# Optimization experiments

Hardware: AMD Instinct MI355X
Metric: run time of the kernel (lower is better)

The kernel has to match this reference:

```python
import jax, jax.numpy as jnp
import numpy as np

N_GENES = 15135
N_CMT = 1000
HID = 64


def _gcn_norm(edge_index, n):
    # add self-loops, compute symmetric normalization deg^-1/2 * deg^-1/2
    loop = jnp.arange(n, dtype=edge_index.dtype)
    src = jnp.concatenate([edge_index[0], loop])
    dst = jnp.concatenate([edge_index[1], loop])
    deg = jax.ops.segment_sum(jnp.ones_like(src, dtype=jnp.float32), dst, num_segments=n)
    dinv = jnp.where(deg > 0, 1.0 / jnp.sqrt(deg), 0.0)
    return src, dst, dinv[src] * dinv[dst]


def _gcn_conv(x, W, b, src, dst, norm, n):
    h = x @ W                                  # [bs, N, H]
    m = h[:, src, :] * norm[None, :, None]     # gather messages [bs, E, H]
    out = jnp.zeros_like(h).at[:, dst, :].add(m)
    return out + b


def setup_inputs():
    key = jax.random.key(0)
    ks = jax.random.split(key, 16)
    bs, nf, hfc, ncls, E, P = 8, 64, 128, 2, 242160, 120000
    s = 0.05
    return {
        "x": jax.random.normal(ks[0], (bs, N_GENES, nf), jnp.float32),
        "batch": jnp.zeros((bs,), jnp.int32),
        "edge_index": jax.random.randint(ks[1], (2, E), 0, N_GENES),
        "path_row": jax.random.randint(ks[2], (P,), 0, N_GENES),
        "path_col": jax.random.randint(ks[3], (P,), 0, N_CMT),
        "W1": jax.random.normal(ks[4], (nf, HID), jnp.float32) * s,
        "b1": jnp.zeros((HID,), jnp.float32),
        "W2": jax.random.normal(ks[5], (HID, HID), jnp.float32) * s,
        "b2": jnp.zeros((HID,), jnp.float32),
        "W3": jax.random.normal(ks[6], (HID, HID), jnp.float32) * s,
        "b3": jnp.zeros((HID,), jnp.float32),
        "fcW": jax.random.normal(ks[7], (3 * HID, 1), jnp.float32) * s,
        "fcb": jnp.zeros((1,), jnp.float32),
        "l1W": jax.random.normal(ks[8], (N_CMT, hfc), jnp.float32) * s,
        "l1b": jnp.zeros((hfc,), jnp.float32),
        "l2W": jax.random.normal(ks[9], (hfc, ncls), jnp.float32) * s,
        "l2b": jnp.zeros((ncls,), jnp.float32),
    }


def reference(x, batch, edge_index, path_row, path_col,
              W1, b1, W2, b2, W3, b3, fcW, fcb, l1W, l1b, l2W, l2b):
    bs, n = x.shape[0], x.shape[1]
    src, dst, norm = _gcn_norm(edge_index, n)

    x1 = jax.nn.relu(_gcn_conv(x, W1, b1, src, dst, norm, n))
    x2 = jax.nn.relu(_gcn_conv(x1, W2, b2, src, dst, norm, n))
    x3 = jax.nn.relu(_gcn_conv(x2, W3, b3, src, dst, norm, n))
    # mode='cat': torch.stack(xs, -1).view(bs, N, -1) -> layout [..., h*L + l]
    xc = jnp.stack([x1, x2, x3], axis=-1).reshape(bs, n, HID * 3)

    # pathway pooling: scatter_mean(x[row], col) over node axis
    xt = jnp.transpose(xc, (1, 0, 2))            # [N, bs, F]
    g = xt[path_row]                             # [P, bs, F]
    sums = jax.ops.segment_sum(g, path_col, num_segments=N_CMT)
    cnt = jax.ops.segment_sum(jnp.ones_like(path_col, dtype=xc.dtype), path_col, num_segments=N_CMT)
    pooled = sums / jnp.maximum(cnt, 1.0)[:, None, None]   # [n_cmt, bs, F]
    pooled = jnp.transpose(pooled, (1, 0, 2)).reshape(-1, HID * 3)  # [bs*n_cmt, F]

    h = (pooled @ fcW + fcb).reshape(bs, N_CMT)   # fc -> view(-1, n_cmt)
    h = jax.nn.relu(h @ l1W + l1b)                # (dropout is identity in eval)
    h = h @ l2W + l2b
    return jax.nn.log_softmax(h, axis=-1)
```

## Files before the change

kernel.cpp:

```cpp
#include <hip/hip_runtime.h>
#include <hip/hip_bf16.h>
#include <hip/hip_fp16.h>
#include <math.h>

#define HID 64

#if defined(__has_builtin)
#if __has_builtin(__builtin_amdgcn_cvt_pk_f32_fp8) && __has_builtin(__builtin_amdgcn_cvt_pk_fp8_f32)
#define HWFP8 1
#endif
#endif

typedef float vfloat2 __attribute__((ext_vector_type(2)));
typedef __attribute__((ext_vector_type(8))) short short8_t;
typedef __attribute__((ext_vector_type(4))) float f32x4;

union ABFrag { short8_t s; unsigned short u[8]; };


__device__ __forceinline__ unsigned short f2bf(float x) {
    unsigned int u = __float_as_uint(x);
    unsigned int r = u + 0x7fffu + ((u >> 16) & 1u);
    return (unsigned short)(r >> 16);
}

#ifndef HWFP8
__device__ __forceinline__ unsigned int enc8_sw(float a) {
    unsigned short hb = __half_as_ushort(__float2half(a));
    unsigned int r = (unsigned int)hb + 0x7fu + ((hb >> 8) & 1u);
    return (r >> 8) & 0xffu;
}
__device__ __forceinline__ float dec8_sw(unsigned int b) {
    return __half2float(__ushort_as_half((unsigned short)(b << 8)));
}
#endif

__device__ __forceinline__ unsigned int enc4(float a, float b, float c, float d) {
#ifdef HWFP8
    int r = __builtin_amdgcn_cvt_pk_fp8_f32(a, b, 0, false);
    r = __builtin_amdgcn_cvt_pk_fp8_f32(c, d, r, true);
    return (unsigned int)r;
#else
    return enc8_sw(a) | (enc8_sw(b) << 8) | (enc8_sw(c) << 16) | (enc8_sw(d) << 24);
#endif
}

__device__ __forceinline__ void dec4(unsigned int w, float* f) {
#ifdef HWFP8
    vfloat2 a = __builtin_amdgcn_cvt_pk_f32_fp8((int)w, false);
    vfloat2 b = __builtin_amdgcn_cvt_pk_f32_fp8((int)w, true);
    f[0] = a.x; f[1] = a.y; f[2] = b.x; f[3] = b.y;
#else
    f[0] = dec8_sw(w & 0xffu); f[1] = dec8_sw((w >> 8) & 0xffu);
    f[2] = dec8_sw((w >> 16) & 0xffu); f[3] = dec8_sw(w >> 24);
#endif
}

__device__ __forceinline__ void dec8(uint2 g, float* f) {
    dec4(g.x, f);
    dec4(g.y, f + 4);
}


__global__ __launch_bounds__(256) void k_pre_count(const int* __restrict__ edst, int* __restrict__ deg, int E,
                                                   const int* __restrict__ pcol, int* __restrict__ ccnt, int P,
                                                   const float* __restrict__ W1, const float* __restrict__ W2,
                                                   const float* __restrict__ W3, unsigned short* __restrict__ Wt) {
    int gth = blockIdx.x * blockDim.x + threadIdx.x;
    int GT = gridDim.x * blockDim.x;
    for (int e = gth; e < E; e += GT) atomicAdd(&deg[edst[e]], 1);
    for (int p = gth; p < P; p += GT) atomicAdd(&ccnt[pcol[p]], 1);
    for (int i = gth; i < 3 * 4096; i += GT) {
        int l = i >> 12, r = i & 4095;
        int k = r >> 6, c = r & 63;
        const float* W = (l == 0) ? W1 : (l == 1) ? W2 : W3;
        Wt[(l << 12) + c * 64 + k] = f2bf(W[r]);
    }
}

__global__ __launch_bounds__(256) void k_pre_scan(const int* __restrict__ deg, int* __restrict__ rowoff, int N,
                                                  const int* __restrict__ ccnt, int* __restrict__ coff, int NC,
                                                  float* __restrict__ dinv) {
    __shared__ int part[256];
    int t = threadIdx.x;
    int gth = blockIdx.x * blockDim.x + t;
    int GT = gridDim.x * blockDim.x;
    for (int i = gth; i < N; i += GT) dinv[i] = rsqrtf((float)(deg[i] + 1));

    const int* cnt = nullptr; int* off = nullptr; int n = 0;
    if (blockIdx.x == 0)      { cnt = deg;  off = rowoff; n = N; }
    else if (blockIdx.x == 1) { cnt = ccnt; off = coff;   n = NC; }
    else return;

    int CH = (n + 255) >> 8;
    int lo = min(t * CH, n), hi = min(lo + CH, n);
    int sum = 0;
    for (int i = lo; i < hi; ++i) sum += cnt[i];
    part[t] = sum;
    __syncthreads();
    for (int o = 1; o < 256; o <<= 1) {
        int v = (t >= o) ? part[t - o] : 0;
        __syncthreads();
        part[t] += v;
        __syncthreads();
    }
    int run = (t == 0) ? 0 : part[t - 1];
    for (int i = lo; i < hi; ++i) { off[i] = run; run += cnt[i]; }
    if (t == 255) off[n] = run;
}

__global__ __launch_bounds__(256) void k_pre_scatter(const int* __restrict__ esrc, const int* __restrict__ edst,
                                                     const float* __restrict__ dinv, const int* __restrict__ rowoff,
                                                     int* __restrict__ fill, int* __restrict__ ssrc,
                                                     float* __restrict__ snorm, int E,
                                                     const int* __restrict__ prow, const int* __restrict__ pcol,
                                                     const int* __restrict__ coff, int* __restrict__ cfill,
                                                     int* __restrict__ crow, int P) {
    int gth = blockIdx.x * blockDim.x + threadIdx.x;
    int GT = gridDim.x * blockDim.x;
    for (int e = gth; e < E; e += GT) {
        int s = esrc[e], d = edst[e];
        int pos = rowoff[d] + atomicAdd(&fill[d], 1);
        ssrc[pos]  = s;
        snorm[pos] = dinv[s] * dinv[d];
    }
    for (int p = gth; p < P; p += GT) {
        int c = pcol[p];
        int pos = coff[c] + atomicAdd(&cfill[c], 1);
        crow[pos] = prow[p];
    }
}


template<int MODE>
__global__ __launch_bounds__(256) void k_gemm_mfma(const void* __restrict__ Xv,
                                                   const unsigned short* __restrict__ Wt,
                                                   unsigned int* __restrict__ Yq,
                                                   float S, int N, int rowsTot) {
    __shared__ float sOut[4][16 * 68];
    int t = threadIdx.x;
    int w = t >> 6, lane = t & 63;
    int r0w = blockIdx.x * 64 + w * 16;
    int rA = r0w + (lane & 15);
    int kg = (lane >> 4) * 8;
    int cc = lane & 15;

    const float* Xf = (const float*)Xv;
    const unsigned short* Xh = (const unsigned short*)Xv;

    f32x4 acc[4] = {f32x4{}, f32x4{}, f32x4{}, f32x4{}};

#pragma unroll
    for (int k0 = 0; k0 < 64; k0 += 32) {
        ABFrag a;
        if (rA < rowsTot) {
            if (MODE == 0) {
                int n = rA >> 3, b = rA & 7;
                const float* p = &Xf[((size_t)b * N + n) * 64 + k0 + kg];
                float4 v0 = *(const float4*)p;
                float4 v1 = *(const float4*)(p + 4);
                a.u[0] = f2bf(v0.x); a.u[1] = f2bf(v0.y);
                a.u[2] = f2bf(v0.z); a.u[3] = f2bf(v0.w);
                a.u[4] = f2bf(v1.x); a.u[5] = f2bf(v1.y);
                a.u[6] = f2bf(v1.z); a.u[7] = f2bf(v1.w);
            } else {
                a.s = *(const short8_t*)&Xh[(size_t)rA * 64 + k0 + kg];
            }
        } else {
#pragma unroll
            for (int j = 0; j < 8; ++j) a.u[j] = 0;
        }
#pragma unroll
        for (int c = 0; c < 4; ++c) {
            ABFrag b;
            b.s = *(const short8_t*)&Wt[(size_t)(c * 16 + cc) * 64 + k0 + kg];
            acc[c] = __builtin_amdgcn_mfma_f32_16x16x32_bf16(a.s, b.s, acc[c], 0, 0, 0);
        }
    }

    float* so = &sOut[w][0];
    int cr = (lane >> 4) * 4;
#pragma unroll
    for (int c = 0; c < 4; ++c) {
        so[(cr + 0) * 68 + c * 16 + cc] = acc[c][0];
        so[(cr + 1) * 68 + c * 16 + cc] = acc[c][1];
        so[(cr + 2) * 68 + c * 16 + cc] = acc[c][2];
        so[(cr + 3) * 68 + c * 16 + cc] = acc[c][3];
    }
    __syncthreads();
#pragma unroll
    for (int i = 0; i < 4; ++i) {
        int idx = lane + i * 64;
        int row = idx >> 4, ci = idx & 15;
        int grow = r0w + row;
        if (grow < rowsTot) {
            float4 v = *(const float4*)&so[row * 68 + ci * 4];
            Yq[(size_t)grow * 16 + ci] =
                enc4(v.x * S, v.y * S, v.z * S, v.w * S);
        }
    }
}

template<int LAYER, bool STORE>
__global__ __launch_bounds__(256) void k_agg(const uint2* __restrict__ Y,
                                             const int* __restrict__ rowoff,
                                             const int* __restrict__ ssrc,
                                             const float* __restrict__ snorm,
                                             const float* __restrict__ dinv,
                                             const float* __restrict__ bias,
                                             const float* __restrict__ fcW,
                                             uint4* __restrict__ O,
                                             float* __restrict__ sArr,
                                             float invS, int N) {
    int n = blockIdx.x * 4 + (threadIdx.x >> 6);
    if (n >= N) return;
    int lane = threadIdx.x & 63;
    int hb = (lane & 7) * 8;
    float bv[8], wv[8];
#pragma unroll
    for (int k = 0; k < 8; ++k) { bv[k] = bias[hb + k]; wv[k] = fcW[3 * (hb + k) + LAYER]; }

    float dn = dinv[n];
    float w0 = dn * dn;
    float acc[8], f[8];
    dec8(Y[(size_t)n * 64 + lane], f);
#pragma unroll
    for (int k = 0; k < 8; ++k) acc[k] = w0 * f[k];

    int beg = rowoff[n], end = rowoff[n + 1];
    int i = beg;
    for (; i + 7 < end; i += 8) {
        int   sI[8];
        float wI[8];
        uint2 g[8];
#pragma unroll
        for (int u = 0; u < 8; ++u) { sI[u] = ssrc[i + u]; wI[u] = snorm[i + u]; }
#pragma unroll
        for (int u = 0; u < 8; ++u) g[u] = Y[(size_t)sI[u] * 64 + lane];
#pragma unroll
        for (int u = 0; u < 8; ++u) {
            dec8(g[u], f);
#pragma unroll
            for (int k = 0; k < 8; ++k) acc[k] = fmaf(wI[u], f[k], acc[k]);
        }
    }
    for (; i < end; ++i) {
        int s = ssrc[i];
        float w = snorm[i];
        dec8(Y[(size_t)s * 64 + lane], f);
#pragma unroll
        for (int k = 0; k < 8; ++k) acc[k] = fmaf(w, f[k], acc[k]);
    }

    float sv = 0.f;
#pragma unroll
    for (int k = 0; k < 8; ++k) {
        float o = fmaxf(fmaf(acc[k], invS, bv[k]), 0.f);
        acc[k] = o;
        sv = fmaf(o, wv[k], sv);
    }
    if (STORE) {
        uint4 o;
        o.x = (unsigned int)f2bf(acc[0]) | ((unsigned int)f2bf(acc[1]) << 16);
        o.y = (unsigned int)f2bf(acc[2]) | ((unsigned int)f2bf(acc[3]) << 16);
        o.z = (unsigned int)f2bf(acc[4]) | ((unsigned int)f2bf(acc[5]) << 16);
        o.w = (unsigned int)f2bf(acc[6]) | ((unsigned int)f2bf(acc[7]) << 16);
        O[(size_t)n * 64 + lane] = o;
    }
    sv += __shfl_down(sv, 4, 64);
    sv += __shfl_down(sv, 2, 64);
    sv += __shfl_down(sv, 1, 64);
    if ((lane & 7) == 0) {
        int b = lane >> 3;
        float* sp = sArr + (size_t)n * 8 + b;
        if (LAYER == 0) *sp = sv;
        else            *sp += sv;
    }
}


__global__ __launch_bounds__(64) void k_poolg(const float* __restrict__ sArr,
                                              const int* __restrict__ coff,
                                              const int* __restrict__ crow,
                                              float* __restrict__ hpoolT) {
    int c = blockIdx.x;
    int lane = threadIdx.x;
    int beg = coff[c], end = coff[c + 1];
    int b = lane & 7;
    float acc = 0.f;
    int i = beg + (lane >> 3);
    for (; i + 24 < end; i += 32) {
        int r0 = crow[i], r1 = crow[i + 8], r2 = crow[i + 16], r3 = crow[i + 24];
        float a0 = sArr[(size_t)r0 * 8 + b];
        float a1 = sArr[(size_t)r1 * 8 + b];
        float a2 = sArr[(size_t)r2 * 8 + b];
        float a3 = sArr[(size_t)r3 * 8 + b];
        acc += (a0 + a1) + (a2 + a3);
    }
    for (; i < end; i += 8) acc += sArr[(size_t)crow[i] * 8 + b];
    acc += __shfl_down(acc, 32, 64);
    acc += __shfl_down(acc, 16, 64);
    acc += __shfl_down(acc, 8, 64);
    if (lane < 8) {
        float inv = 1.f / fmaxf((float)(end - beg), 1.f);
        hpoolT[(size_t)c * 8 + b] = acc * inv;
    }
}

__global__ __launch_bounds__(128) void k_l1f(const float* __restrict__ hpoolT,
                                             const float* __restrict__ fcb,
                                             const float* __restrict__ l1W,
                                             float* __restrict__ hpre,
                                             int* __restrict__ done,
                                             const float* __restrict__ l1b,
                                             const float* __restrict__ l2W,
                                             const float* __restrict__ l2b,
                                             float* __restrict__ out,
                                             int NC, int HFC, int bs, int NCLS,
                                             int CHUNK, int nBlocks) {
    __shared__ float hl[64];
    int b = blockIdx.y;
    int c0 = blockIdx.x * CHUNK;
    int j = threadIdx.x;
    int cend = min(c0 + CHUNK, NC);
    for (int c = c0 + j; c < cend; c += blockDim.x)
        hl[c - c0] = hpoolT[(size_t)c * 8 + b] + fcb[0];
    __syncthreads();
    float acc = 0.f;
    for (int c = c0; c < cend; ++c) acc = fmaf(hl[c - c0], l1W[(size_t)c * HFC + j], acc);
    atomicAdd(&hpre[(size_t)b * HFC + j], acc);

    __threadfence();
    __syncthreads();
    __shared__ int amLast;
    if (j == 0) amLast = (atomicAdd(done, 1) == nBlocks - 1);
    __syncthreads();
    if (!amLast) return;
    __threadfence();

    __shared__ float sZ[64];
    int g = j >> 3, l8 = j & 7;
    int nout = bs * NCLS;
    float v = 0.f;
    int b2 = g / NCLS, k2 = g - b2 * NCLS;
    if (g < nout) {
        for (int jj = l8; jj < HFC; jj += 8) {
            float h = fmaxf(hpre[(size_t)b2 * HFC + jj] + l1b[jj], 0.f);
            v = fmaf(h, l2W[(size_t)jj * NCLS + k2], v);
        }
    }
    v += __shfl_down(v, 4, 8);
    v += __shfl_down(v, 2, 8);
    v += __shfl_down(v, 1, 8);
    if (l8 == 0 && g < nout) sZ[g] = v + l2b[k2];
    __syncthreads();
    if (j < bs) {
        float m = -1e30f;
        for (int c = 0; c < NCLS; ++c) m = fmaxf(m, sZ[j * NCLS + c]);
        float s = 0.f;
        for (int c = 0; c < NCLS; ++c) s += expf(sZ[j * NCLS + c] - m);
        float lse = m + logf(s);
        for (int c = 0; c < NCLS; ++c) out[j * NCLS + c] = sZ[j * NCLS + c] - lse;
    }
}


extern "C" void kernel_launch(void* const* d_in, const int* in_sizes, int n_in,
                              void* d_out, int out_size, void* d_ws, size_t ws_size,
                              hipStream_t stream) {
    const float* x   = (const float*)d_in[0];
    const int* eidx  = (const int*)d_in[2];
    const int* prow  = (const int*)d_in[3];
    const int* pcol  = (const int*)d_in[4];
    const float* W1  = (const float*)d_in[5];
    const float* b1  = (const float*)d_in[6];
    const float* W2  = (const float*)d_in[7];
    const float* b2  = (const float*)d_in[8];
    const float* W3  = (const float*)d_in[9];
    const float* b3  = (const float*)d_in[10];
    const float* fcW = (const float*)d_in[11];
    const float* fcb = (const float*)d_in[12];
    const float* l1W = (const float*)d_in[13];
    const float* l1b = (const float*)d_in[14];
    const float* l2W = (const float*)d_in[15];
    const float* l2b = (const float*)d_in[16];
    float* out = (float*)d_out;

    const int bs   = in_sizes[1];
    const int E    = in_sizes[2] / 2;
    const int P    = in_sizes[3];
    const int N    = in_sizes[0] / (bs * HID);
    const int HFC  = in_sizes[14];
    const int NC   = in_sizes[13] / HFC;
    const int NCLS = in_sizes[15] / HFC;
    const int rows = N * bs;

    const int* esrc = eidx;
    const int* edst = eidx + E;

    size_t off = 0;
    auto alloc = [&](size_t bytes) -> void* {
        void* r = (char*)d_ws + off;
        off += (bytes + 255) & ~(size_t)255;
        return r;
    };
    char* zbase   = (char*)d_ws;
    int*   deg    = (int*)  alloc((size_t)N * 4);
    int*   fill   = (int*)  alloc((size_t)N * 4);
    int*   ccnt   = (int*)  alloc((size_t)NC * 4);
    int*   cfill  = (int*)  alloc((size_t)NC * 4);
    float* hpre   = (float*)alloc((size_t)bs * HFC * 4);
    int*   done   = (int*)  alloc(4);
    size_t zspan  = off;
    float* dinv   = (float*)alloc((size_t)N * 4);
    int*   rowoff = (int*)  alloc(((size_t)N + 1) * 4);
    int*   coff   = (int*)  alloc(((size_t)NC + 1) * 4);
    int*   crow   = (int*)  alloc((size_t)P * 4);
    float* hpoolT = (float*)alloc((size_t)NC * bs * 4);
    int*   ssrc   = (int*)  alloc((size_t)E * 4);
    float* snorm  = (float*)alloc((size_t)E * 4);
    unsigned int* Yq   = (unsigned int*)alloc((size_t)rows * HID);
    unsigned short* X1 = (unsigned short*)alloc((size_t)rows * HID * 2);
    unsigned short* X2 = (unsigned short*)alloc((size_t)rows * HID * 2);
    float* sArr   = (float*)alloc((size_t)rows * 4);
    unsigned short* Wt = (unsigned short*)alloc((size_t)3 * 64 * 64 * 2);

    hipMemsetAsync(zbase, 0, zspan, stream);

    int gPre = 512;
    k_pre_count<<<gPre, 256, 0, stream>>>(edst, deg, E, pcol, ccnt, P, W1, W2, W3, Wt);
    k_pre_scan<<<64, 256, 0, stream>>>(deg, rowoff, N, ccnt, coff, NC, dinv);
    k_pre_scatter<<<gPre, 256, 0, stream>>>(esrc, edst, dinv, rowoff, fill, ssrc, snorm, E,
                                            prow, pcol, coff, cfill, crow, P);

    const float S1 = 1.f,  iS1 = 1.f;
    const float S2 = 16.f, iS2 = 1.f / 16.f;
    const float S3 = 128.f, iS3 = 1.f / 128.f;

    int gG = (rows + 63) / 64;
    int gA = (N + 3) / 4;
    k_gemm_mfma<0><<<gG, 256, 0, stream>>>(x, Wt, Yq, S1, N, rows);
    k_agg<0, true><<<gA, 256, 0, stream>>>((const uint2*)Yq, rowoff, ssrc, snorm, dinv, b1, fcW, (uint4*)X1, sArr, iS1, N);
    k_gemm_mfma<1><<<gG, 256, 0, stream>>>(X1, Wt + 4096, Yq, S2, N, rows);
    k_agg<1, true><<<gA, 256, 0, stream>>>((const uint2*)Yq, rowoff, ssrc, snorm, dinv, b2, fcW, (uint4*)X2, sArr, iS2, N);
    k_gemm_mfma<1><<<gG, 256, 0, stream>>>(X2, Wt + 8192, Yq, S3, N, rows);
    k_agg<2, false><<<gA, 256, 0, stream>>>((const uint2*)Yq, rowoff, ssrc, snorm, dinv, b3, fcW, nullptr, sArr, iS3, N);

    k_poolg<<<NC, 64, 0, stream>>>(sArr, coff, crow, hpoolT);

    const int CHUNK = 40;
    dim3 gL1((NC + CHUNK - 1) / CHUNK, bs);
    int nBlocks = gL1.x * gL1.y;
    k_l1f<<<gL1, 128, 0, stream>>>(hpoolT, fcb, l1W, hpre, done, l1b, l2W, l2b, out,
                                   NC, HFC, bs, NCLS, CHUNK, nBlocks);
}
```

Before: 361.1 us.

## Fuse whole pipeline into one cooperative persistent kernel with grid syncs

Replaces the chain of separate launches (preprocessing count/scan/scatter, three GEMM and aggregation layers, pooling, MLP head) with one cooperative kernel that uses grid.sync between phases and grid-stride loops over tiles. The goal is to remove per-launch overhead and the idle gaps between many small kernels. The trade-offs are that each grid barrier has its own cost, the scan phases now run on only two blocks, and the persistent grid of at most 1024 blocks may give less parallelism or occupancy than the original launches. If the cooperative launch fails, the code falls back to the old multi-kernel path.

```diff
diff --git a/kernel.cpp b/kernel.cpp
--- a/kernel.cpp
+++ b/kernel.cpp
@@ -1,7 +1,10 @@
 #include <hip/hip_runtime.h>
+#include <hip/hip_cooperative_groups.h>
 #include <hip/hip_bf16.h>
 #include <hip/hip_fp16.h>
 #include <math.h>
+
+namespace cg = cooperative_groups;
 
 #define HID 64
 
@@ -59,6 +62,332 @@
 __device__ __forceinline__ void dec8(uint2 g, float* f) {
     dec4(g.x, f);
     dec4(g.y, f + 4);
+}
+
+
+struct MegaArgs {
+    const float* x;
+    const int* esrc; const int* edst;
+    const int* prow; const int* pcol;
+    const float* W1; const float* W2; const float* W3;
+    const float* b1; const float* b2; const float* b3;
+    const float* fcW; const float* fcb;
+    const float* l1W; const float* l1b;
+    const float* l2W; const float* l2b;
+    float* out;
+    int* deg; int* fill; int* ccnt; int* cfill;
+    float* hpre; float* dinv;
+    int* rowoff; int* coff; int* crow;
+    float* hpoolT; int* ssrc; float* snorm;
+    unsigned int* Yq; unsigned short* X1; unsigned short* X2;
+    float* sArr; unsigned short* Wt;
+    int N, E, P, NC, HFC, bs, NCLS, rows;
+};
+
+template<int MODE>
+__device__ __forceinline__ void gemm_phase(float* sOutAll, const void* Xv,
+                                           const unsigned short* Wt,
+                                           unsigned int* Yq, float S,
+                                           int N, int rowsTot,
+                                           int bid, int nB, int tid) {
+    int w = tid >> 6, lane = tid & 63;
+    int nT = (rowsTot + 63) >> 6;
+    const float* Xf = (const float*)Xv;
+    const unsigned short* Xh = (const unsigned short*)Xv;
+    float* so = sOutAll + w * (16 * 68);
+    int cc = lane & 15;
+    int kg = (lane >> 4) * 8;
+    int cr = (lane >> 4) * 4;
+
+    for (int tile = bid; tile < nT; tile += nB) {
+        int r0w = tile * 64 + w * 16;
+        int rA = r0w + (lane & 15);
+        f32x4 acc[4] = {f32x4{}, f32x4{}, f32x4{}, f32x4{}};
+#pragma unroll
+        for (int k0 = 0; k0 < 64; k0 += 32) {
+            ABFrag a;
+            if (rA < rowsTot) {
+                if (MODE == 0) {
+                    int n = rA >> 3, b = rA & 7;
+                    const float* p = &Xf[((size_t)b * N + n) * 64 + k0 + kg];
+                    float4 v0 = *(const float4*)p;
+                    float4 v1 = *(const float4*)(p + 4);
+                    a.u[0] = f2bf(v0.x); a.u[1] = f2bf(v0.y);
+                    a.u[2] = f2bf(v0.z); a.u[3] = f2bf(v0.w);
+                    a.u[4] = f2bf(v1.x); a.u[5] = f2bf(v1.y);
+                    a.u[6] = f2bf(v1.z); a.u[7] = f2bf(v1.w);
+                } else {
+                    a.s = *(const short8_t*)&Xh[(size_t)rA * 64 + k0 + kg];
+                }
+            } else {
+#pragma unroll
+                for (int j = 0; j < 8; ++j) a.u[j] = 0;
+            }
+#pragma unroll
+            for (int c = 0; c < 4; ++c) {
+                ABFrag b;
+                b.s = *(const short8_t*)&Wt[(size_t)(c * 16 + cc) * 64 + k0 + kg];
+                acc[c] = __builtin_amdgcn_mfma_f32_16x16x32_bf16(a.s, b.s, acc[c], 0, 0, 0);
+            }
+        }
+#pragma unroll
+        for (int c = 0; c < 4; ++c) {
+            so[(cr + 0) * 68 + c * 16 + cc] = acc[c][0];
+            so[(cr + 1) * 68 + c * 16 + cc] = acc[c][1];
+            so[(cr + 2) * 68 + c * 16 + cc] = acc[c][2];
+            so[(cr + 3) * 68 + c * 16 + cc] = acc[c][3];
+        }
+        __syncthreads();
+#pragma unroll
+        for (int i = 0; i < 4; ++i) {
+            int idx = lane + i * 64;
+            int row = idx >> 4, ci = idx & 15;
+            int grow = r0w + row;
+            if (grow < rowsTot) {
+                float4 v = *(const float4*)&so[row * 68 + ci * 4];
+                Yq[(size_t)grow * 16 + ci] =
+                    enc4(v.x * S, v.y * S, v.z * S, v.w * S);
+            }
+        }
+        __syncthreads();
+    }
+}
+
+template<int LAYER, bool STORE>
+__device__ __forceinline__ void agg_phase(const uint2* Y, const int* rowoff,
+                                          const int* ssrc, const float* snorm,
+                                          const float* dinv, const float* bias,
+                                          const float* fcW, uint4* O, float* sArr,
+                                          float invS, int N,
+                                          int bid, int nB, int tid) {
+    int w = tid >> 6, lane = tid & 63;
+    int nG = (N + 3) >> 2;
+    int hb = (lane & 7) * 8;
+    float bv[8], wv[8];
+#pragma unroll
+    for (int k = 0; k < 8; ++k) { bv[k] = bias[hb + k]; wv[k] = fcW[3 * (hb + k) + LAYER]; }
+
+    for (int g = bid; g < nG; g += nB) {
+        int n = g * 4 + w;
+        if (n < N) {
+            float dn = dinv[n];
+            float w0 = dn * dn;
+            float acc[8], f[8];
+            dec8(Y[(size_t)n * 64 + lane], f);
+#pragma unroll
+            for (int k = 0; k < 8; ++k) acc[k] = w0 * f[k];
+
+            int beg = rowoff[n], end = rowoff[n + 1];
+            int i = beg;
+            for (; i + 7 < end; i += 8) {
+                int   sI[8];
+                float wI[8];
+                uint2 gg[8];
+#pragma unroll
+                for (int u = 0; u < 8; ++u) { sI[u] = ssrc[i + u]; wI[u] = snorm[i + u]; }
+#pragma unroll
+                for (int u = 0; u < 8; ++u) gg[u] = Y[(size_t)sI[u] * 64 + lane];
+#pragma unroll
+                for (int u = 0; u < 8; ++u) {
+                    dec8(gg[u], f);
+#pragma unroll
+                    for (int k = 0; k < 8; ++k) acc[k] = fmaf(wI[u], f[k], acc[k]);
+                }
+            }
+            for (; i < end; ++i) {
+                int s = ssrc[i];
+                float ww = snorm[i];
+                dec8(Y[(size_t)s * 64 + lane], f);
+#pragma unroll
+                for (int k = 0; k < 8; ++k) acc[k] = fmaf(ww, f[k], acc[k]);
+            }
+
+            float sv = 0.f;
+#pragma unroll
+            for (int k = 0; k < 8; ++k) {
+                float o = fmaxf(fmaf(acc[k], invS, bv[k]), 0.f);
+                acc[k] = o;
+                sv = fmaf(o, wv[k], sv);
+            }
+            if (STORE) {
+                uint4 o;
+                o.x = (unsigned int)f2bf(acc[0]) | ((unsigned int)f2bf(acc[1]) << 16);
+                o.y = (unsigned int)f2bf(acc[2]) | ((unsigned int)f2bf(acc[3]) << 16);
+                o.z = (unsigned int)f2bf(acc[4]) | ((unsigned int)f2bf(acc[5]) << 16);
+                o.w = (unsigned int)f2bf(acc[6]) | ((unsigned int)f2bf(acc[7]) << 16);
+                O[(size_t)n * 64 + lane] = o;
+            }
+            sv += __shfl_down(sv, 4, 64);
+            sv += __shfl_down(sv, 2, 64);
+            sv += __shfl_down(sv, 1, 64);
+            if ((lane & 7) == 0) {
+                int b = lane >> 3;
+                float* sp = sArr + (size_t)n * 8 + b;
+                if (LAYER == 0) *sp = sv;
+                else            *sp += sv;
+            }
+        }
+    }
+}
+
+union SmemU {
+    float sOut[4 * 16 * 68];
+    int   part[256];
+    float hl2[2][64];
+    float sZ[64];
+};
+
+__global__ __launch_bounds__(256, 4) void k_mega(MegaArgs A) {
+    cg::grid_group grid = cg::this_grid();
+    __shared__ SmemU sm;
+    int tid = threadIdx.x;
+    int bid = blockIdx.x;
+    int nB  = gridDim.x;
+    int GT  = nB * 256;
+    int gth = bid * 256 + tid;
+    int w = tid >> 6, lane = tid & 63;
+
+    for (int e = gth; e < A.E; e += GT) atomicAdd(&A.deg[A.edst[e]], 1);
+    for (int p = gth; p < A.P; p += GT) atomicAdd(&A.ccnt[A.pcol[p]], 1);
+    for (int i = gth; i < 3 * 4096; i += GT) {
+        int l = i >> 12, r = i & 4095;
+        int k = r >> 6, c = r & 63;
+        const float* W = (l == 0) ? A.W1 : (l == 1) ? A.W2 : A.W3;
+        A.Wt[(l << 12) + c * 64 + k] = f2bf(W[r]);
+    }
+    grid.sync();
+
+    for (int i = gth; i < A.N; i += GT) A.dinv[i] = rsqrtf((float)(A.deg[i] + 1));
+    if (bid < 2) {
+        const int* cnt; int* off; int n;
+        if (bid == 0) { cnt = A.deg;  off = A.rowoff; n = A.N; }
+        else          { cnt = A.ccnt; off = A.coff;   n = A.NC; }
+        int t = tid;
+        int CH = (n + 255) >> 8;
+        int lo = min(t * CH, n), hi = min(lo + CH, n);
+        int sum = 0;
+        for (int i = lo; i < hi; ++i) sum += cnt[i];
+        sm.part[t] = sum;
+        __syncthreads();
+        for (int o = 1; o < 256; o <<= 1) {
+            int v = (t >= o) ? sm.part[t - o] : 0;
+            __syncthreads();
+            sm.part[t] += v;
+            __syncthreads();
+        }
+        int run = (t == 0) ? 0 : sm.part[t - 1];
+        for (int i = lo; i < hi; ++i) { off[i] = run; run += cnt[i]; }
+        if (t == 255) off[n] = run;
+    }
+    grid.sync();
+
+    for (int e = gth; e < A.E; e += GT) {
+        int s = A.esrc[e], d = A.edst[e];
+        int pos = A.rowoff[d] + atomicAdd(&A.fill[d], 1);
+        A.ssrc[pos]  = s;
+        A.snorm[pos] = A.dinv[s] * A.dinv[d];
+    }
+    for (int p = gth; p < A.P; p += GT) {
+        int c = A.pcol[p];
+        int pos = A.coff[c] + atomicAdd(&A.cfill[c], 1);
+        A.crow[pos] = A.prow[p];
+    }
+    grid.sync();
+
+    const float S1 = 1.f,   iS1 = 1.f;
+    const float S2 = 16.f,  iS2 = 1.f / 16.f;
+    const float S3 = 128.f, iS3 = 1.f / 128.f;
+
+    gemm_phase<0>(sm.sOut, A.x, A.Wt, A.Yq, S1, A.N, A.rows, bid, nB, tid);
+    grid.sync();
+    agg_phase<0, true>((const uint2*)A.Yq, A.rowoff, A.ssrc, A.snorm, A.dinv, A.b1, A.fcW,
+                       (uint4*)A.X1, A.sArr, iS1, A.N, bid, nB, tid);
+    grid.sync();
+    gemm_phase<1>(sm.sOut, A.X1, A.Wt + 4096, A.Yq, S2, A.N, A.rows, bid, nB, tid);
+    grid.sync();
+    agg_phase<1, true>((const uint2*)A.Yq, A.rowoff, A.ssrc, A.snorm, A.dinv, A.b2, A.fcW,
+                       (uint4*)A.X2, A.sArr, iS2, A.N, bid, nB, tid);
+    grid.sync();
+    gemm_phase<1>(sm.sOut, A.X2, A.Wt + 8192, A.Yq, S3, A.N, A.rows, bid, nB, tid);
+    grid.sync();
+    agg_phase<2, false>((const uint2*)A.Yq, A.rowoff, A.ssrc, A.snorm, A.dinv, A.b3, A.fcW,
+                        nullptr, A.sArr, iS3, A.N, bid, nB, tid);
+    grid.sync();
+
+    for (int c = bid * 4 + w; c < A.NC; c += nB * 4) {
+        int beg = A.coff[c], end = A.coff[c + 1];
+        int b = lane & 7;
+        float acc = 0.f;
+        int i = beg + (lane >> 3);
+        for (; i + 24 < end; i += 32) {
+            int r0 = A.crow[i], r1 = A.crow[i + 8], r2 = A.crow[i + 16], r3 = A.crow[i + 24];
+            float a0 = A.sArr[(size_t)r0 * 8 + b];
+            float a1 = A.sArr[(size_t)r1 * 8 + b];
+            float a2 = A.sArr[(size_t)r2 * 8 + b];
+            float a3 = A.sArr[(size_t)r3 * 8 + b];
+            acc += (a0 + a1) + (a2 + a3);
+        }
+        for (; i < end; i += 8) acc += A.sArr[(size_t)A.crow[i] * 8 + b];
+        acc += __shfl_down(acc, 32, 64);
+        acc += __shfl_down(acc, 16, 64);
+        acc += __shfl_down(acc, 8, 64);
+        if (lane < 8) {
+            float inv = 1.f / fmaxf((float)(end - beg), 1.f);
+            A.hpoolT[(size_t)c * 8 + b] = acc * inv;
+        }
+    }
+    grid.sync();
+
+    {
+        const int CHUNK = 40;
+        int gx25 = (A.NC + CHUNK - 1) / CHUNK;
+        int nJobs = gx25 * A.bs;
+        int h = tid >> 7, j = tid & 127;
+        float fcb0 = A.fcb[0];
+        for (int jj = bid * 2; jj < nJobs; jj += nB * 2) {
+            int J = jj + h;
+            int gx = J % gx25, b = J / gx25;
+            int c0 = gx * CHUNK;
+            int cend = min(c0 + CHUNK, A.NC);
+            float* hl = sm.hl2[h];
+            for (int c = c0 + j; c < cend; c += 128)
+                hl[c - c0] = A.hpoolT[(size_t)c * 8 + b] + fcb0;
+            __syncthreads();
+            float acc = 0.f;
+            for (int c = c0; c < cend; ++c)
+                acc = fmaf(hl[c - c0], A.l1W[(size_t)c * A.HFC + j], acc);
+            atomicAdd(&A.hpre[(size_t)b * A.HFC + j], acc);
+            __syncthreads();
+        }
+    }
+    grid.sync();
+
+    if (bid == 0) {
+        int j = tid;
+        int g = j >> 3, l8 = j & 7;
+        int nout = A.bs * A.NCLS;
+        float v = 0.f;
+        int b2 = g / A.NCLS, k2 = g - b2 * A.NCLS;
+        if (g < nout) {
+            for (int jj2 = l8; jj2 < A.HFC; jj2 += 8) {
+                float hh = fmaxf(A.hpre[(size_t)b2 * A.HFC + jj2] + A.l1b[jj2], 0.f);
+                v = fmaf(hh, A.l2W[(size_t)jj2 * A.NCLS + k2], v);
+            }
+        }
+        v += __shfl_down(v, 4, 8);
+        v += __shfl_down(v, 2, 8);
+        v += __shfl_down(v, 1, 8);
+        if (l8 == 0 && g < nout) sm.sZ[g] = v + A.l2b[k2];
+        __syncthreads();
+        if (j < A.bs) {
+            float m = -1e30f;
+            for (int c = 0; c < A.NCLS; ++c) m = fmaxf(m, sm.sZ[j * A.NCLS + c]);
+            float s = 0.f;
+            for (int c = 0; c < A.NCLS; ++c) s += expf(sm.sZ[j * A.NCLS + c] - m);
+            float lse = m + logf(s);
+            for (int c = 0; c < A.NCLS; ++c) A.out[j * A.NCLS + c] = sm.sZ[j * A.NCLS + c] - lse;
+        }
+    }
 }
 
 
@@ -131,74 +460,13 @@
     }
 }
 
-
 template<int MODE>
 __global__ __launch_bounds__(256) void k_gemm_mfma(const void* __restrict__ Xv,
                                                    const unsigned short* __restrict__ Wt,
                                                    unsigned int* __restrict__ Yq,
                                                    float S, int N, int rowsTot) {
     __shared__ float sOut[4][16 * 68];
-    int t = threadIdx.x;
-    int w = t >> 6, lane = t & 63;
-    int r0w = blockIdx.x * 64 + w * 16;
-    int rA = r0w + (lane & 15);
-    int kg = (lane >> 4) * 8;
-    int cc = lane & 15;
-
-    const float* Xf = (const float*)Xv;
-    const unsigned short* Xh = (const unsigned short*)Xv;
-
-    f32x4 acc[4] = {f32x4{}, f32x4{}, f32x4{}, f32x4{}};
-
-#pragma unroll
-    for (int k0 = 0; k0 < 64; k0 += 32) {
-        ABFrag a;
-        if (rA < rowsTot) {
-            if (MODE == 0) {
-                int n = rA >> 3, b = rA & 7;
-                const float* p = &Xf[((size_t)b * N + n) * 64 + k0 + kg];
-                float4 v0 = *(const float4*)p;
-                float4 v1 = *(const float4*)(p + 4);
-                a.u[0] = f2bf(v0.x); a.u[1] = f2bf(v0.y);
-                a.u[2] = f2bf(v0.z); a.u[3] = f2bf(v0.w);
-                a.u[4] = f2bf(v1.x); a.u[5] = f2bf(v1.y);
-                a.u[6] = f2bf(v1.z); a.u[7] = f2bf(v1.w);
-            } else {
-                a.s = *(const short8_t*)&Xh[(size_t)rA * 64 + k0 + kg];
-            }
-        } else {
-#pragma unroll
-            for (int j = 0; j < 8; ++j) a.u[j] = 0;
-        }
-#pragma unroll
-        for (int c = 0; c < 4; ++c) {
-            ABFrag b;
-            b.s = *(const short8_t*)&Wt[(size_t)(c * 16 + cc) * 64 + k0 + kg];
-            acc[c] = __builtin_amdgcn_mfma_f32_16x16x32_bf16(a.s, b.s, acc[c], 0, 0, 0);
-        }
-    }
-
-    float* so = &sOut[w][0];
-    int cr = (lane >> 4) * 4;
-#pragma unroll
-    for (int c = 0; c < 4; ++c) {
-        so[(cr + 0) * 68 + c * 16 + cc] = acc[c][0];
-        so[(cr + 1) * 68 + c * 16 + cc] = acc[c][1];
-        so[(cr + 2) * 68 + c * 16 + cc] = acc[c][2];
-        so[(cr + 3) * 68 + c * 16 + cc] = acc[c][3];
-    }
-    __syncthreads();
-#pragma unroll
-    for (int i = 0; i < 4; ++i) {
-        int idx = lane + i * 64;
-        int row = idx >> 4, ci = idx & 15;
-        int grow = r0w + row;
-        if (grow < rowsTot) {
-            float4 v = *(const float4*)&so[row * 68 + ci * 4];
-            Yq[(size_t)grow * 16 + ci] =
-                enc4(v.x * S, v.y * S, v.z * S, v.w * S);
-        }
-    }
+    gemm_phase<MODE>(&sOut[0][0], Xv, Wt, Yq, S, N, rowsTot, blockIdx.x, gridDim.x, threadIdx.x);
 }
 
 template<int LAYER, bool STORE>
@@ -212,72 +480,9 @@
                                              uint4* __restrict__ O,
                                              float* __restrict__ sArr,
                                              float invS, int N) {
-    int n = blockIdx.x * 4 + (threadIdx.x >> 6);
-    if (n >= N) return;
-    int lane = threadIdx.x & 63;
-    int hb = (lane & 7) * 8;
-    float bv[8], wv[8];
-#pragma unroll
-    for (int k = 0; k < 8; ++k) { bv[k] = bias[hb + k]; wv[k] = fcW[3 * (hb + k) + LAYER]; }
-
-    float dn = dinv[n];
-    float w0 = dn * dn;
-    float acc[8], f[8];
-    dec8(Y[(size_t)n * 64 + lane], f);
-#pragma unroll
-    for (int k = 0; k < 8; ++k) acc[k] = w0 * f[k];
-
-    int beg = rowoff[n], end = rowoff[n + 1];
-    int i = beg;
-    for (; i + 7 < end; i += 8) {
-        int   sI[8];
-        float wI[8];
-        uint2 g[8];
-#pragma unroll
-        for (int u = 0; u < 8; ++u) { sI[u] = ssrc[i + u]; wI[u] = snorm[i + u]; }
-#pragma unroll
-        for (int u = 0; u < 8; ++u) g[u] = Y[(size_t)sI[u] * 64 + lane];
-#pragma unroll
-        for (int u = 0; u < 8; ++u) {
-            dec8(g[u], f);
-#pragma unroll
-            for (int k = 0; k < 8; ++k) acc[k] = fmaf(wI[u], f[k], acc[k]);
-        }
-    }
-    for (; i < end; ++i) {
-        int s = ssrc[i];
-        float w = snorm[i];
-        dec8(Y[(size_t)s * 64 + lane], f);
-#pragma unroll
-        for (int k = 0; k < 8; ++k) acc[k] = fmaf(w, f[k], acc[k]);
-    }
-
-    float sv = 0.f;
-#pragma unroll
-    for (int k = 0; k < 8; ++k) {
-        float o = fmaxf(fmaf(acc[k], invS, bv[k]), 0.f);
-        acc[k] = o;
-        sv = fmaf(o, wv[k], sv);
-    }
-    if (STORE) {
-        uint4 o;
-        o.x = (unsigned int)f2bf(acc[0]) | ((unsigned int)f2bf(acc[1]) << 16);
-        o.y = (unsigned int)f2bf(acc[2]) | ((unsigned int)f2bf(acc[3]) << 16);
-        o.z = (unsigned int)f2bf(acc[4]) | ((unsigned int)f2bf(acc[5]) << 16);
-        o.w = (unsigned int)f2bf(acc[6]) | ((unsigned int)f2bf(acc[7]) << 16);
-        O[(size_t)n * 64 + lane] = o;
-    }
-    sv += __shfl_down(sv, 4, 64);
-    sv += __shfl_down(sv, 2, 64);
-    sv += __shfl_down(sv, 1, 64);
-    if ((lane & 7) == 0) {
-        int b = lane >> 3;
-        float* sp = sArr + (size_t)n * 8 + b;
-        if (LAYER == 0) *sp = sv;
-        else            *sp += sv;
-    }
-}
-
+    agg_phase<LAYER, STORE>(Y, rowoff, ssrc, snorm, dinv, bias, fcW, O, sArr, invS, N,
+                            blockIdx.x, gridDim.x, threadIdx.x);
+}
 
 __global__ __launch_bounds__(64) void k_poolg(const float* __restrict__ sArr,
                                               const int* __restrict__ coff,
@@ -427,6 +632,29 @@
 
     hipMemsetAsync(zbase, 0, zspan, stream);
 
+    MegaArgs A;
+    A.x = x; A.esrc = esrc; A.edst = edst; A.prow = prow; A.pcol = pcol;
+    A.W1 = W1; A.W2 = W2; A.W3 = W3; A.b1 = b1; A.b2 = b2; A.b3 = b3;
+    A.fcW = fcW; A.fcb = fcb; A.l1W = l1W; A.l1b = l1b; A.l2W = l2W; A.l2b = l2b;
+    A.out = out;
+    A.deg = deg; A.fill = fill; A.ccnt = ccnt; A.cfill = cfill;
+    A.hpre = hpre; A.dinv = dinv; A.rowoff = rowoff; A.coff = coff; A.crow = crow;
+    A.hpoolT = hpoolT; A.ssrc = ssrc; A.snorm = snorm;
+    A.Yq = Yq; A.X1 = X1; A.X2 = X2; A.sArr = sArr; A.Wt = Wt;
+    A.N = N; A.E = E; A.P = P; A.NC = NC; A.HFC = HFC; A.bs = bs; A.NCLS = NCLS; A.rows = rows;
+
+    int maxB = 0;
+    hipError_t occErr = hipOccupancyMaxActiveBlocksPerMultiprocessor(&maxB, k_mega, 256, 0);
+    if (occErr != hipSuccess || maxB < 1) maxB = 1;
+    int nB = maxB * 256;
+    if (nB > 1024) nB = 1024;
+    if (nB < 2) nB = 2;
+
+    void* kargs[] = { (void*)&A };
+    hipError_t err = hipLaunchCooperativeKernel((const void*)k_mega, dim3(nB), dim3(256),
+                                                kargs, 0, stream);
+    if (err == hipSuccess) return;
+
     int gPre = 512;
     k_pre_count<<<gPre, 256, 0, stream>>>(edst, deg, E, pcol, ccnt, P, W1, W2, W3, Wt);
     k_pre_scan<<<64, 256, 0, stream>>>(deg, rowoff, N, ccnt, coff, NC, dinv);
```

New measurement: 984.8 us. 173% more time.

## Fuse layer-1 GEMM with preprocessing and fold pooling into L1 kernel

Applied to the files above, without the earlier changes.

The layer-1 GEMM, which depends only on x and W1, now runs in the same launch as the degree and count atomics and the W2/W3 transpose. It uses extra blocks and reads W1 directly with on-the-fly bf16 conversion. The pathway mean-pooling kernel is removed and its work moves into the first FC kernel, where each 16-lane group pools one pathway into shared memory. This cuts two kernel launches and the hpoolT round trip, but pooling is now repeated per batch-column block, and W1 is loaded strided and uncached-transposed per block.

```diff
diff --git a/kernel.cpp b/kernel.cpp
--- a/kernel.cpp
+++ b/kernel.cpp
@@ -61,22 +61,146 @@
     dec4(g.y, f + 4);
 }
 
-
-__global__ __launch_bounds__(256) void k_pre_count(const int* __restrict__ edst, int* __restrict__ deg, int E,
-                                                   const int* __restrict__ pcol, int* __restrict__ ccnt, int P,
-                                                   const float* __restrict__ W1, const float* __restrict__ W2,
-                                                   const float* __restrict__ W3, unsigned short* __restrict__ Wt) {
-    int gth = blockIdx.x * blockDim.x + threadIdx.x;
-    int GT = gridDim.x * blockDim.x;
-    for (int e = gth; e < E; e += GT) atomicAdd(&deg[edst[e]], 1);
-    for (int p = gth; p < P; p += GT) atomicAdd(&ccnt[pcol[p]], 1);
-    for (int i = gth; i < 3 * 4096; i += GT) {
-        int l = i >> 12, r = i & 4095;
-        int k = r >> 6, c = r & 63;
-        const float* W = (l == 0) ? W1 : (l == 1) ? W2 : W3;
-        Wt[(l << 12) + c * 64 + k] = f2bf(W[r]);
-    }
-}
+__device__ __forceinline__ void gemm_bf16_phase(float* so4, const unsigned short* Xh,
+                                                const unsigned short* Wt,
+                                                unsigned int* Yq, float S,
+                                                int rowsTot, int tile, int tid) {
+    int w = tid >> 6, lane = tid & 63;
+    float* so = so4 + w * (16 * 68);
+    int cc = lane & 15;
+    int kg = (lane >> 4) * 8;
+    int cr = (lane >> 4) * 4;
+    int r0w = tile * 64 + w * 16;
+    int rA = r0w + (lane & 15);
+    f32x4 acc[4] = {f32x4{}, f32x4{}, f32x4{}, f32x4{}};
+#pragma unroll
+    for (int k0 = 0; k0 < 64; k0 += 32) {
+        ABFrag a;
+        if (rA < rowsTot) {
+            a.s = *(const short8_t*)&Xh[(size_t)rA * 64 + k0 + kg];
+        } else {
+#pragma unroll
+            for (int j = 0; j < 8; ++j) a.u[j] = 0;
+        }
+#pragma unroll
+        for (int c = 0; c < 4; ++c) {
+            ABFrag b;
+            b.s = *(const short8_t*)&Wt[(size_t)(c * 16 + cc) * 64 + k0 + kg];
+            acc[c] = __builtin_amdgcn_mfma_f32_16x16x32_bf16(a.s, b.s, acc[c], 0, 0, 0);
+        }
+    }
+#pragma unroll
+    for (int c = 0; c < 4; ++c) {
+        so[(cr + 0) * 68 + c * 16 + cc] = acc[c][0];
+        so[(cr + 1) * 68 + c * 16 + cc] = acc[c][1];
+        so[(cr + 2) * 68 + c * 16 + cc] = acc[c][2];
+        so[(cr + 3) * 68 + c * 16 + cc] = acc[c][3];
+    }
+    __syncthreads();
+#pragma unroll
+    for (int i = 0; i < 4; ++i) {
+        int idx = lane + i * 64;
+        int row = idx >> 4, ci = idx & 15;
+        int grow = r0w + row;
+        if (grow < rowsTot) {
+            float4 v = *(const float4*)&so[row * 68 + ci * 4];
+            Yq[(size_t)grow * 16 + ci] =
+                enc4(v.x * S, v.y * S, v.z * S, v.w * S);
+        }
+    }
+}
+
+template<int DUMMY>
+__global__ __launch_bounds__(256) void k_gemm_mfma(const unsigned short* __restrict__ Xh,
+                                                   const unsigned short* __restrict__ Wt,
+                                                   unsigned int* __restrict__ Yq,
+                                                   float S, int rowsTot) {
+    __shared__ float sOut[4][16 * 68];
+    gemm_bf16_phase(&sOut[0][0], Xh, Wt, Yq, S, rowsTot, blockIdx.x, threadIdx.x);
+}
+
+__global__ __launch_bounds__(256) void k_fused1(const float* __restrict__ x,
+                                                const float* __restrict__ W1,
+                                                unsigned int* __restrict__ Yq,
+                                                float S, int N, int rowsTot, int gG,
+                                                const int* __restrict__ edst, int* __restrict__ deg, int E,
+                                                const int* __restrict__ pcol, int* __restrict__ ccnt, int P,
+                                                const float* __restrict__ W2, const float* __restrict__ W3,
+                                                unsigned short* __restrict__ Wt) {
+    __shared__ float sOut[4][16 * 68];
+    int tid = threadIdx.x;
+    if ((int)blockIdx.x < gG) {
+        int w = tid >> 6, lane = tid & 63;
+        float* so = &sOut[w][0];
+        int cc = lane & 15;
+        int kg = (lane >> 4) * 8;
+        int cr = (lane >> 4) * 4;
+        int r0w = blockIdx.x * 64 + w * 16;
+        int rA = r0w + (lane & 15);
+        ABFrag a[2];
+#pragma unroll
+        for (int h = 0; h < 2; ++h) {
+            if (rA < rowsTot) {
+                int n = rA >> 3, b = rA & 7;
+                const float* p = &x[((size_t)b * N + n) * 64 + h * 32 + kg];
+                float4 v0 = *(const float4*)p;
+                float4 v1 = *(const float4*)(p + 4);
+                a[h].u[0] = f2bf(v0.x); a[h].u[1] = f2bf(v0.y);
+                a[h].u[2] = f2bf(v0.z); a[h].u[3] = f2bf(v0.w);
+                a[h].u[4] = f2bf(v1.x); a[h].u[5] = f2bf(v1.y);
+                a[h].u[6] = f2bf(v1.z); a[h].u[7] = f2bf(v1.w);
+            } else {
+#pragma unroll
+                for (int j = 0; j < 8; ++j) a[h].u[j] = 0;
+            }
+        }
+        f32x4 acc[4] = {f32x4{}, f32x4{}, f32x4{}, f32x4{}};
+#pragma unroll
+        for (int h = 0; h < 2; ++h) {
+#pragma unroll
+            for (int c = 0; c < 4; ++c) {
+                ABFrag b;
+#pragma unroll
+                for (int j = 0; j < 8; ++j)
+                    b.u[j] = f2bf(W1[(size_t)(h * 32 + kg + j) * 64 + c * 16 + cc]);
+                acc[c] = __builtin_amdgcn_mfma_f32_16x16x32_bf16(a[h].s, b.s, acc[c], 0, 0, 0);
+            }
+        }
+#pragma unroll
+        for (int c = 0; c < 4; ++c) {
+            so[(cr + 0) * 68 + c * 16 + cc] = acc[c][0];
+            so[(cr + 1) * 68 + c * 16 + cc] = acc[c][1];
+            so[(cr + 2) * 68 + c * 16 + cc] = acc[c][2];
+            so[(cr + 3) * 68 + c * 16 + cc] = acc[c][3];
+        }
+        __syncthreads();
+#pragma unroll
+        for (int i = 0; i < 4; ++i) {
+            int idx = lane + i * 64;
+            int row = idx >> 4, ci = idx & 15;
+            int grow = r0w + row;
+            if (grow < rowsTot) {
+                float4 v = *(const float4*)&so[row * 68 + ci * 4];
+                Yq[(size_t)grow * 16 + ci] =
+                    enc4(v.x * S, v.y * S, v.z * S, v.w * S);
+            }
+        }
+    } else {
+        int cb = blockIdx.x - gG;
+        int nCB = gridDim.x - gG;
+        int gth = cb * 256 + tid;
+        int GT = nCB * 256;
+        for (int e = gth; e < E; e += GT) atomicAdd(&deg[edst[e]], 1);
+        for (int p = gth; p < P; p += GT) atomicAdd(&ccnt[pcol[p]], 1);
+        for (int i = gth; i < 2 * 4096; i += GT) {
+            int l = i >> 12, r = i & 4095;
+            int k = r >> 6, c = r & 63;
+            const float* W = (l == 0) ? W2 : W3;
+            Wt[(l << 12) + c * 64 + k] = f2bf(W[r]);
+        }
+    }
+}
+
 
 __global__ __launch_bounds__(256) void k_pre_scan(const int* __restrict__ deg, int* __restrict__ rowoff, int N,
                                                   const int* __restrict__ ccnt, int* __restrict__ coff, int NC,
@@ -131,75 +255,6 @@
     }
 }
 
-
-template<int MODE>
-__global__ __launch_bounds__(256) void k_gemm_mfma(const void* __restrict__ Xv,
-                                                   const unsigned short* __restrict__ Wt,
-                                                   unsigned int* __restrict__ Yq,
-                                                   float S, int N, int rowsTot) {
-    __shared__ float sOut[4][16 * 68];
-    int t = threadIdx.x;
-    int w = t >> 6, lane = t & 63;
-    int r0w = blockIdx.x * 64 + w * 16;
-    int rA = r0w + (lane & 15);
-    int kg = (lane >> 4) * 8;
-    int cc = lane & 15;
-
-    const float* Xf = (const float*)Xv;
-    const unsigned short* Xh = (const unsigned short*)Xv;
-
-    f32x4 acc[4] = {f32x4{}, f32x4{}, f32x4{}, f32x4{}};
-
-#pragma unroll
-    for (int k0 = 0; k0 < 64; k0 += 32) {
-        ABFrag a;
-        if (rA < rowsTot) {
-            if (MODE == 0) {
-                int n = rA >> 3, b = rA & 7;
-                const float* p = &Xf[((size_t)b * N + n) * 64 + k0 + kg];
-                float4 v0 = *(const float4*)p;
-                float4 v1 = *(const float4*)(p + 4);
-                a.u[0] = f2bf(v0.x); a.u[1] = f2bf(v0.y);
-                a.u[2] = f2bf(v0.z); a.u[3] = f2bf(v0.w);
-                a.u[4] = f2bf(v1.x); a.u[5] = f2bf(v1.y);
-                a.u[6] = f2bf(v1.z); a.u[7] = f2bf(v1.w);
-            } else {
-                a.s = *(const short8_t*)&Xh[(size_t)rA * 64 + k0 + kg];
-            }
-        } else {
-#pragma unroll
-            for (int j = 0; j < 8; ++j) a.u[j] = 0;
-        }
-#pragma unroll
-        for (int c = 0; c < 4; ++c) {
-            ABFrag b;
-            b.s = *(const short8_t*)&Wt[(size_t)(c * 16 + cc) * 64 + k0 + kg];
-            acc[c] = __builtin_amdgcn_mfma_f32_16x16x32_bf16(a.s, b.s, acc[c], 0, 0, 0);
-        }
-    }
-
-    float* so = &sOut[w][0];
-    int cr = (lane >> 4) * 4;
-#pragma unroll
-    for (int c = 0; c < 4; ++c) {
-        so[(cr + 0) * 68 + c * 16 + cc] = acc[c][0];
-        so[(cr + 1) * 68 + c * 16 + cc] = acc[c][1];
-        so[(cr + 2) * 68 + c * 16 + cc] = acc[c][2];
-        so[(cr + 3) * 68 + c * 16 + cc] = acc[c][3];
-    }
-    __syncthreads();
-#pragma unroll
-    for (int i = 0; i < 4; ++i) {
-        int idx = lane + i * 64;
-        int row = idx >> 4, ci = idx & 15;
-        int grow = r0w + row;
-        if (grow < rowsTot) {
-            float4 v = *(const float4*)&so[row * 68 + ci * 4];
-            Yq[(size_t)grow * 16 + ci] =
-                enc4(v.x * S, v.y * S, v.z * S, v.w * S);
-        }
-    }
-}
 
 template<int LAYER, bool STORE>
 __global__ __launch_bounds__(256) void k_agg(const uint2* __restrict__ Y,
@@ -278,53 +333,40 @@
     }
 }
 
-
-__global__ __launch_bounds__(64) void k_poolg(const float* __restrict__ sArr,
-                                              const int* __restrict__ coff,
-                                              const int* __restrict__ crow,
-                                              float* __restrict__ hpoolT) {
-    int c = blockIdx.x;
-    int lane = threadIdx.x;
-    int beg = coff[c], end = coff[c + 1];
-    int b = lane & 7;
-    float acc = 0.f;
-    int i = beg + (lane >> 3);
-    for (; i + 24 < end; i += 32) {
-        int r0 = crow[i], r1 = crow[i + 8], r2 = crow[i + 16], r3 = crow[i + 24];
-        float a0 = sArr[(size_t)r0 * 8 + b];
-        float a1 = sArr[(size_t)r1 * 8 + b];
-        float a2 = sArr[(size_t)r2 * 8 + b];
-        float a3 = sArr[(size_t)r3 * 8 + b];
-        acc += (a0 + a1) + (a2 + a3);
-    }
-    for (; i < end; i += 8) acc += sArr[(size_t)crow[i] * 8 + b];
-    acc += __shfl_down(acc, 32, 64);
-    acc += __shfl_down(acc, 16, 64);
-    acc += __shfl_down(acc, 8, 64);
-    if (lane < 8) {
-        float inv = 1.f / fmaxf((float)(end - beg), 1.f);
-        hpoolT[(size_t)c * 8 + b] = acc * inv;
-    }
-}
-
-__global__ __launch_bounds__(128) void k_l1f(const float* __restrict__ hpoolT,
-                                             const float* __restrict__ fcb,
-                                             const float* __restrict__ l1W,
-                                             float* __restrict__ hpre,
-                                             int* __restrict__ done,
-                                             const float* __restrict__ l1b,
-                                             const float* __restrict__ l2W,
-                                             const float* __restrict__ l2b,
-                                             float* __restrict__ out,
-                                             int NC, int HFC, int bs, int NCLS,
-                                             int CHUNK, int nBlocks) {
+__global__ __launch_bounds__(128) void k_l1pool(const float* __restrict__ sArr,
+                                                const int* __restrict__ coff,
+                                                const int* __restrict__ crow,
+                                                const float* __restrict__ fcb,
+                                                const float* __restrict__ l1W,
+                                                float* __restrict__ hpre,
+                                                int* __restrict__ done,
+                                                const float* __restrict__ l1b,
+                                                const float* __restrict__ l2W,
+                                                const float* __restrict__ l2b,
+                                                float* __restrict__ out,
+                                                int NC, int HFC, int bs, int NCLS,
+                                                int CHUNK, int nBlocks) {
     __shared__ float hl[64];
     int b = blockIdx.y;
     int c0 = blockIdx.x * CHUNK;
     int j = threadIdx.x;
     int cend = min(c0 + CHUNK, NC);
-    for (int c = c0 + j; c < cend; c += blockDim.x)
-        hl[c - c0] = hpoolT[(size_t)c * 8 + b] + fcb[0];
+    {
+        int w = j >> 6, lane = j & 63, q = lane >> 4, s = lane & 15;
+        float fcb0 = fcb[0];
+        for (int c = c0 + w * 4 + q; c < cend; c += 8) {
+            int beg = coff[c], end = coff[c + 1];
+            float acc = 0.f;
+            for (int i = beg + s; i < end; i += 16)
+                acc += sArr[(size_t)crow[i] * 8 + b];
+            acc += __shfl_down(acc, 8, 16);
+            acc += __shfl_down(acc, 4, 16);
+            acc += __shfl_down(acc, 2, 16);
+            acc += __shfl_down(acc, 1, 16);
+            if (s == 0)
+                hl[c - c0] = acc / fmaxf((float)(end - beg), 1.f) + fcb0;
+        }
+    }
     __syncthreads();
     float acc = 0.f;
     for (int c = c0; c < cend; ++c) acc = fmaf(hl[c - c0], l1W[(size_t)c * HFC + j], acc);
@@ -416,41 +458,39 @@
     int*   rowoff = (int*)  alloc(((size_t)N + 1) * 4);
     int*   coff   = (int*)  alloc(((size_t)NC + 1) * 4);
     int*   crow   = (int*)  alloc((size_t)P * 4);
-    float* hpoolT = (float*)alloc((size_t)NC * bs * 4);
     int*   ssrc   = (int*)  alloc((size_t)E * 4);
     float* snorm  = (float*)alloc((size_t)E * 4);
     unsigned int* Yq   = (unsigned int*)alloc((size_t)rows * HID);
     unsigned short* X1 = (unsigned short*)alloc((size_t)rows * HID * 2);
     unsigned short* X2 = (unsigned short*)alloc((size_t)rows * HID * 2);
     float* sArr   = (float*)alloc((size_t)rows * 4);
-    unsigned short* Wt = (unsigned short*)alloc((size_t)3 * 64 * 64 * 2);
+    unsigned short* Wt = (unsigned short*)alloc((size_t)2 * 64 * 64 * 2);
 
     hipMemsetAsync(zbase, 0, zspan, stream);
 
+    const float S1 = 1.f,  iS1 = 1.f;
+    const float S2 = 16.f, iS2 = 1.f / 16.f;
+    const float S3 = 128.f, iS3 = 1.f / 128.f;
+
+    int gG = (rows + 63) / 64;
+    int gA = (N + 3) / 4;
     int gPre = 512;
-    k_pre_count<<<gPre, 256, 0, stream>>>(edst, deg, E, pcol, ccnt, P, W1, W2, W3, Wt);
+
+    k_fused1<<<gG + gPre, 256, 0, stream>>>(x, W1, Yq, S1, N, rows, gG,
+                                            edst, deg, E, pcol, ccnt, P, W2, W3, Wt);
     k_pre_scan<<<64, 256, 0, stream>>>(deg, rowoff, N, ccnt, coff, NC, dinv);
     k_pre_scatter<<<gPre, 256, 0, stream>>>(esrc, edst, dinv, rowoff, fill, ssrc, snorm, E,
                                             prow, pcol, coff, cfill, crow, P);
 
-    const float S1 = 1.f,  iS1 = 1.f;
-    const float S2 = 16.f, iS2 = 1.f / 16.f;
-    const float S3 = 128.f, iS3 = 1.f / 128.f;
-
-    int gG = (rows + 63) / 64;
-    int gA = (N + 3) / 4;
-    k_gemm_mfma<0><<<gG, 256, 0, stream>>>(x, Wt, Yq, S1, N, rows);
     k_agg<0, true><<<gA, 256, 0, stream>>>((const uint2*)Yq, rowoff, ssrc, snorm, dinv, b1, fcW, (uint4*)X1, sArr, iS1, N);
-    k_gemm_mfma<1><<<gG, 256, 0, stream>>>(X1, Wt + 4096, Yq, S2, N, rows);
+    k_gemm_mfma<0><<<gG, 256, 0, stream>>>(X1, Wt, Yq, S2, rows);
     k_agg<1, true><<<gA, 256, 0, stream>>>((const uint2*)Yq, rowoff, ssrc, snorm, dinv, b2, fcW, (uint4*)X2, sArr, iS2, N);
-    k_gemm_mfma<1><<<gG, 256, 0, stream>>>(X2, Wt + 8192, Yq, S3, N, rows);
+    k_gemm_mfma<0><<<gG, 256, 0, stream>>>(X2, Wt + 4096, Yq, S3, rows);
     k_agg<2, false><<<gA, 256, 0, stream>>>((const uint2*)Yq, rowoff, ssrc, snorm, dinv, b3, fcW, nullptr, sArr, iS3, N);
-
-    k_poolg<<<NC, 64, 0, stream>>>(sArr, coff, crow, hpoolT);
 
     const int CHUNK = 40;
     dim3 gL1((NC + CHUNK - 1) / CHUNK, bs);
     int nBlocks = gL1.x * gL1.y;
-    k_l1f<<<gL1, 128, 0, stream>>>(hpoolT, fcb, l1W, hpre, done, l1b, l2W, l2b, out,
-                                   NC, HFC, bs, NCLS, CHUNK, nBlocks);
-}
+    k_l1pool<<<gL1, 128, 0, stream>>>(sArr, coff, crow, fcb, l1W, hpre, done,
+                                      l1b, l2W, l2b, out, NC, HFC, bs, NCLS, CHUNK, nBlocks);
+}
```

Measured after the change: 368.1 us. About the same (+1.9%).
